# Kernel tuning notes

Measured on AMD Instinct MI355X. Metric: run time of the kernel, lower is better.

The kernel has to match this reference:

```python
import jax, jax.numpy as jnp
import numpy as np

EPS = 0.5  # diffusion epsilon from init_kwargs

def setup_inputs() -> dict:
    key = jax.random.key(0)
    k = jax.random.split(key, 7)
    B, N0, N1, n = 1024, 32, 32, 64
    Mu0 = jax.random.normal(k[0], (N0, n), dtype=jnp.float32) * 2.0
    Mu1 = jax.random.normal(k[1], (N1, n), dtype=jnp.float32) * 2.0
    # diagonal covariances must be positive
    S0 = jax.random.uniform(k[2], (N0, n), dtype=jnp.float32, minval=0.1, maxval=1.0)
    S1 = jax.random.uniform(k[3], (N1, n), dtype=jnp.float32, minval=0.1, maxval=1.0)
    Lam = jax.random.uniform(k[4], (N0, N1), dtype=jnp.float32, minval=0.0, maxval=1.0)
    Lam = Lam / Lam.sum()  # transport plan sums to 1
    X = jax.random.normal(k[5], (B, n), dtype=jnp.float32)
    t = jnp.float32(0.3)
    return {"X": X, "Mu0": Mu0, "Mu1": Mu1, "S0": S0, "S1": S1, "Lam": Lam, "t": t}

def reference(X, Mu0, Mu1, S0, S1, Lam, t):
    eps2 = EPS * EPS
    S0e = S0[:, None, :]        # (N0,1,n)
    S1e = S1[None, :, :]        # (1,N1,n)
    Ds = jnp.sqrt(4.0 * S0e * S1e + EPS ** 4)
    Cs = 0.5 * (Ds - eps2)                       # (N0,N1,n)
    mu_t = (1.0 - t) * Mu0[:, None, :] + t * Mu1[None, :, :]  # (N0,N1,n)
    Sigma = (1.0 - t) ** 2 * S0e + t ** 2 * S1e + 2.0 * t * (1.0 - t) * (Cs + 0.5 * eps2)
    # St = Pt - Qt - eps^2 * t
    St = t * S1e + (1.0 - t) * Cs - ((1.0 - t) * S0e + t * Cs) - eps2 * t
    K = St / Sigma                               # (N0,N1,n)
    v = Mu1[None, :, :] - Mu0[:, None, :]        # (N0,N1,n)
    d = X[:, None, None, :] - mu_t               # (B,N0,N1,n)
    U = K * d + v                                # (B,N0,N1,n)
    # diag-Normal log_prob plus n/2*log(2pi) == -0.5*sum(d^2/Sigma + log Sigma)
    logw = -0.5 * jnp.sum(d * d / Sigma + jnp.log(Sigma), axis=-1)  # (B,N0,N1)
    W = jnp.exp(jnp.clip(logw, -50.0, 50.0)) * Lam                  # (B,N0,N1)
    num = jnp.einsum('bijn,bij->bn', U, W)       # (B,n)
    den = jnp.sum(W, axis=(1, 2))[:, None]       # (B,1)
    return num / den
```

## Files before the change

### kernel.cpp

```cpp
#include <hip/hip_runtime.h>
#include <math.h>

#define EPS2f 0.25f
#define EPS4f 0.0625f

__device__ __forceinline__ float rl(float v, int l) {
    return __int_as_float(__builtin_amdgcn_readlane(__float_as_int(v), l));
}

__global__ __launch_bounds__(256) void precomp_kernel(
    const float* __restrict__ Mu0, const float* __restrict__ Mu1,
    const float* __restrict__ S0,  const float* __restrict__ S1,
    const float* __restrict__ tptr,
    float2* __restrict__ AB2, float2* __restrict__ KV2,
    float* __restrict__ C0)
{
    __shared__ float2 abS[4][67];
    __shared__ float2 kvS[4][64];

    const int tid = threadIdx.x;
    const int k   = tid & 63;
    const int ijl = tid >> 6;
    const int ij0 = blockIdx.x << 2;
    const int ij  = ij0 + ijl;
    const int i   = ij >> 5;
    const int j   = ij & 31;
    const float t   = *tptr;
    const float omt = 1.0f - t;

    const float s0 = S0[i * 64 + k];
    const float s1 = S1[j * 64 + k];
    const float m0 = Mu0[i * 64 + k];
    const float m1 = Mu1[j * 64 + k];

    const float ds  = sqrtf(4.0f * s0 * s1 + EPS4f);
    const float cs  = 0.5f * (ds - EPS2f);
    const float mt  = omt * m0 + t * m1;
    const float sig = omt * omt * s0 + t * t * s1
                    + 2.0f * t * omt * (cs + 0.5f * EPS2f);
    const float isig = 1.0f / sig;
    const float st = t * s1 - omt * s0 + (omt - t) * cs - EPS2f * t;
    const float kk = st * isig;
    const float v  = m1 - m0;

    abS[ijl][k] = make_float2(isig, 2.0f * mt * isig);
    kvS[ijl][k] = make_float2(kk, v - kk * mt);

    float c = mt * mt * isig + __logf(sig);
    #pragma unroll
    for (int off = 32; off >= 1; off >>= 1)
        c += __shfl_xor(c, off, 64);
    if (k == 0) C0[ij] = c;

    __syncthreads();

    {
        const int k2   = tid >> 3;
        const int ijl2 = (tid >> 1) & 3;
        const int par  = tid & 1;
        AB2[(k2 << 11) + ((ij0 + ijl2) << 1) + par] = abS[ijl2][2 * k2 + par];
    }
    {
        const int pr  = tid >> 7;
        const int k6  = (tid >> 1) & 63;
        const int par = tid & 1;
        KV2[(blockIdx.x << 8) + tid] = kvS[(pr << 1) + par][k6];
    }
}

__global__ __launch_bounds__(256) void gmm_main_kernel(
    const float* __restrict__ X,   const float* __restrict__ Lam,
    const float* __restrict__ C0,
    const float4* __restrict__ AB4, const float4* __restrict__ KV4,
    float* __restrict__ nump, float* __restrict__ denp)
{
    const int tid    = threadIdx.x;
    const int lane   = tid & 63;
    const int rowsub = tid >> 6;
    const int bx     = blockIdx.x;
    const int c      = bx & 15;
    const int g      = bx >> 4;
    const int r0     = (g << 5) + (rowsub << 3);
    const int ij     = (c << 6) + lane;

    float xr[8];
    #pragma unroll
    for (int u = 0; u < 8; ++u) xr[u] = X[(r0 + u) * 64 + lane];

    const float c0 = C0[ij];
    const float lm = Lam[ij];

    const float4* __restrict__ abp = AB4 + ij;
    float4 ab[4];
    #pragma unroll
    for (int pf = 0; pf < 4; ++pf) ab[pf] = abp[pf << 10];

    float q[8] = {0.f, 0.f, 0.f, 0.f, 0.f, 0.f, 0.f, 0.f};
    #pragma unroll
    for (int k2 = 0; k2 < 32; ++k2) {
        const float4 a = ab[k2 & 3];
        if (k2 + 4 < 32) ab[k2 & 3] = abp[(k2 + 4) << 10];
        #pragma unroll
        for (int u = 0; u < 8; ++u) {
            const float xe = rl(xr[u], 2 * k2);
            const float xo = rl(xr[u], 2 * k2 + 1);
            q[u] = fmaf(fmaf(a.x, xe, -a.y), xe, q[u]);
            q[u] = fmaf(fmaf(a.z, xo, -a.w), xo, q[u]);
        }
    }

    float wv[8];
    #pragma unroll
    for (int u = 0; u < 8; ++u)
        wv[u] = __expf(fminf(fmaxf(-0.5f * (q[u] + c0), -50.f), 50.f)) * lm;

    const float4* __restrict__ kvp = KV4 + (c << 11) + lane;
    float4 kvb[4];
    #pragma unroll
    for (int pf = 0; pf < 4; ++pf) kvb[pf] = kvp[pf << 6];

    float dsum[8];
    #pragma unroll
    for (int u = 0; u < 8; ++u) dsum[u] = wv[u];
    #pragma unroll
    for (int off = 32; off >= 1; off >>= 1) {
        #pragma unroll
        for (int u = 0; u < 8; ++u) dsum[u] += __shfl_xor(dsum[u], off, 64);
    }

    float nacc[8] = {0.f, 0.f, 0.f, 0.f, 0.f, 0.f, 0.f, 0.f};
    #pragma unroll
    for (int p = 0; p < 32; ++p) {
        const float4 kv = kvb[p & 3];
        if (p + 4 < 32) kvb[p & 3] = kvp[(p + 4) << 6];
        #pragma unroll
        for (int u = 0; u < 8; ++u) {
            const float We = rl(wv[u], 2 * p);
            const float Wo = rl(wv[u], 2 * p + 1);
            const float ue = fmaf(kv.x, xr[u], kv.y);
            nacc[u] = fmaf(We, ue, nacc[u]);
            const float uo = fmaf(kv.z, xr[u], kv.w);
            nacc[u] = fmaf(Wo, uo, nacc[u]);
        }
    }

    #pragma unroll
    for (int u = 0; u < 8; ++u)
        nump[(c * 1024 + r0 + u) * 64 + lane] = nacc[u];

    float dv = dsum[0];
    #pragma unroll
    for (int u = 1; u < 8; ++u) dv = (lane == u) ? dsum[u] : dv;
    if (lane < 8) denp[(c << 10) + r0 + lane] = dv;
}

__global__ __launch_bounds__(256) void combine_kernel(
    const float* __restrict__ nump, const float* __restrict__ denp,
    float* __restrict__ out)
{
    const int idx = blockIdx.x * 256 + threadIdx.x;
    const int b = idx >> 6;
    const int k = idx & 63;
    float s = 0.f, d = 0.f;
    #pragma unroll
    for (int c = 0; c < 16; ++c) {
        s += nump[(c * 1024 + b) * 64 + k];
        d += denp[(c << 10) + b];
    }
    out[idx] = s / d;
}

extern "C" void kernel_launch(void* const* d_in, const int* in_sizes, int n_in,
                              void* d_out, int out_size, void* d_ws, size_t ws_size,
                              hipStream_t stream) {
    const float* X   = (const float*)d_in[0];
    const float* Mu0 = (const float*)d_in[1];
    const float* Mu1 = (const float*)d_in[2];
    const float* S0  = (const float*)d_in[3];
    const float* S1  = (const float*)d_in[4];
    const float* Lam = (const float*)d_in[5];
    const float* t   = (const float*)d_in[6];
    float* out = (float*)d_out;

    char* ws = (char*)d_ws;
    float2* AB2  = (float2*)(ws);
    float2* KV2  = (float2*)(ws + (512 << 10));
    float*  C0   = (float*)(ws + (1024 << 10));
    float*  nump = (float*)(ws + (2 << 20));
    float*  denp = (float*)(ws + (6 << 20));

    precomp_kernel<<<256, 256, 0, stream>>>(Mu0, Mu1, S0, S1, t, AB2, KV2, C0);
    gmm_main_kernel<<<512, 256, 0, stream>>>(X, Lam, C0,
                                             (const float4*)AB2,
                                             (const float4*)KV2, nump, denp);
    combine_kernel<<<256, 256, 0, stream>>>(nump, denp, out);
}
```

Baseline: 85.81 us.

## Fuse precompute, main, and combine kernels into one with last-block reduction

Merges the three launches into a single kernel. Each block recomputes its 64 (i,j) component parameters directly into LDS instead of reading them from a global precompute buffer. The cross-chunk reduction is done by the last block to arrive per row group, tracked with an atomic counter that a memset clears before launch. This removes two kernel launches and the global round trips for AB/KV/C0. In exchange, each parameter set is recomputed by 32 blocks, LDS use grows, and a memset plus threadfence/atomic synchronisation are added.

Result: slower. 144.3 us (+68.2%).

```diff
diff --git a/kernel.cpp b/kernel.cpp
--- a/kernel.cpp
+++ b/kernel.cpp
@@ -8,98 +8,93 @@
     return __int_as_float(__builtin_amdgcn_readlane(__float_as_int(v), l));
 }
 
-__global__ __launch_bounds__(256) void precomp_kernel(
-    const float* __restrict__ Mu0, const float* __restrict__ Mu1,
-    const float* __restrict__ S0,  const float* __restrict__ S1,
+__global__ __launch_bounds__(256, 2) void gmm_chunk_kernel(
+    const float* __restrict__ X,   const float* __restrict__ Mu0,
+    const float* __restrict__ Mu1, const float* __restrict__ S0,
+    const float* __restrict__ S1,  const float* __restrict__ Lam,
     const float* __restrict__ tptr,
-    float2* __restrict__ AB2, float2* __restrict__ KV2,
-    float* __restrict__ C0)
+    float* __restrict__ nump, float* __restrict__ denp,
+    unsigned int* __restrict__ ctr, float* __restrict__ out)
 {
-    __shared__ float2 abS[4][67];
-    __shared__ float2 kvS[4][64];
+    __shared__ float4 abL[32][65];
+    __shared__ float4 kvL[32][65];
+    __shared__ float  c0L[64];
+    __shared__ int    lastFlag;
 
-    const int tid = threadIdx.x;
-    const int k   = tid & 63;
-    const int ijl = tid >> 6;
-    const int ij0 = blockIdx.x << 2;
-    const int ij  = ij0 + ijl;
-    const int i   = ij >> 5;
-    const int j   = ij & 31;
+    const int tid  = threadIdx.x;
+    const int lane = tid & 63;
+    const int w    = tid >> 6;
+    const int g    = blockIdx.x >> 4;
+    const int c    = blockIdx.x & 15;
+    const int r0   = (g << 5) + (w << 3);
+
+    const int m   = tid & 31;
+    const int ijb = (tid >> 5) << 3;
     const float t   = *tptr;
     const float omt = 1.0f - t;
 
-    const float s0 = S0[i * 64 + k];
-    const float s1 = S1[j * 64 + k];
-    const float m0 = Mu0[i * 64 + k];
-    const float m1 = Mu1[j * 64 + k];
-
-    const float ds  = sqrtf(4.0f * s0 * s1 + EPS4f);
-    const float cs  = 0.5f * (ds - EPS2f);
-    const float mt  = omt * m0 + t * m1;
-    const float sig = omt * omt * s0 + t * t * s1
-                    + 2.0f * t * omt * (cs + 0.5f * EPS2f);
-    const float isig = 1.0f / sig;
-    const float st = t * s1 - omt * s0 + (omt - t) * cs - EPS2f * t;
-    const float kk = st * isig;
-    const float v  = m1 - m0;
-
-    abS[ijl][k] = make_float2(isig, 2.0f * mt * isig);
-    kvS[ijl][k] = make_float2(kk, v - kk * mt);
-
-    float c = mt * mt * isig + __logf(sig);
+    float Kr[8][2], Vr[8][2], cpart[8];
     #pragma unroll
-    for (int off = 32; off >= 1; off >>= 1)
-        c += __shfl_xor(c, off, 64);
-    if (k == 0) C0[ij] = c;
-
-    __syncthreads();
-
-    {
-        const int k2   = tid >> 3;
-        const int ijl2 = (tid >> 1) & 3;
-        const int par  = tid & 1;
-        AB2[(k2 << 11) + ((ij0 + ijl2) << 1) + par] = abS[ijl2][2 * k2 + par];
+    for (int v = 0; v < 8; ++v) {
+        const int ij = (c << 6) + ijb + v;
+        const int i  = ij >> 5;
+        const int j  = ij & 31;
+        float4 abv;
+        float  csum = 0.f;
+        #pragma unroll
+        for (int r = 0; r < 2; ++r) {
+            const int k  = 2 * m + r;
+            const float s0 = S0[i * 64 + k];
+            const float s1 = S1[j * 64 + k];
+            const float m0 = Mu0[i * 64 + k];
+            const float m1 = Mu1[j * 64 + k];
+            const float dsq = sqrtf(4.0f * s0 * s1 + EPS4f);
+            const float cs  = 0.5f * (dsq - EPS2f);
+            const float mt  = omt * m0 + t * m1;
+            const float sig = omt * omt * s0 + t * t * s1
+                            + 2.0f * t * omt * (cs + 0.5f * EPS2f);
+            const float isig = 1.0f / sig;
+            const float st  = t * s1 - omt * s0 + (omt - t) * cs - EPS2f * t;
+            const float kk  = st * isig;
+            const float vm  = (m1 - m0) - kk * mt;
+            if (r == 0) { abv.x = isig; abv.y = 2.0f * mt * isig; }
+            else        { abv.z = isig; abv.w = 2.0f * mt * isig; }
+            Kr[v][r] = kk; Vr[v][r] = vm;
+            csum += mt * mt * isig + __logf(sig);
+        }
+        abL[m][ijb + v] = abv;
+        cpart[v] = csum;
     }
-    {
-        const int pr  = tid >> 7;
-        const int k6  = (tid >> 1) & 63;
-        const int par = tid & 1;
-        KV2[(blockIdx.x << 8) + tid] = kvS[(pr << 1) + par][k6];
+    #pragma unroll
+    for (int qq = 0; qq < 4; ++qq) {
+        kvL[(ijb >> 1) + qq][2 * m] =
+            make_float4(Kr[2 * qq][0], Vr[2 * qq][0],
+                        Kr[2 * qq + 1][0], Vr[2 * qq + 1][0]);
+        kvL[(ijb >> 1) + qq][2 * m + 1] =
+            make_float4(Kr[2 * qq][1], Vr[2 * qq][1],
+                        Kr[2 * qq + 1][1], Vr[2 * qq + 1][1]);
     }
-}
-
-__global__ __launch_bounds__(256) void gmm_main_kernel(
-    const float* __restrict__ X,   const float* __restrict__ Lam,
-    const float* __restrict__ C0,
-    const float4* __restrict__ AB4, const float4* __restrict__ KV4,
-    float* __restrict__ nump, float* __restrict__ denp)
-{
-    const int tid    = threadIdx.x;
-    const int lane   = tid & 63;
-    const int rowsub = tid >> 6;
-    const int bx     = blockIdx.x;
-    const int c      = bx & 15;
-    const int g      = bx >> 4;
-    const int r0     = (g << 5) + (rowsub << 3);
-    const int ij     = (c << 6) + lane;
+    #pragma unroll
+    for (int v = 0; v < 8; ++v) {
+        float cc = cpart[v];
+        #pragma unroll
+        for (int off = 16; off >= 1; off >>= 1)
+            cc += __shfl_xor(cc, off, 64);
+        if (m == 0) c0L[ijb + v] = cc;
+    }
 
     float xr[8];
     #pragma unroll
     for (int u = 0; u < 8; ++u) xr[u] = X[(r0 + u) * 64 + lane];
 
-    const float c0 = C0[ij];
-    const float lm = Lam[ij];
+    __syncthreads();
 
-    const float4* __restrict__ abp = AB4 + ij;
-    float4 ab[4];
-    #pragma unroll
-    for (int pf = 0; pf < 4; ++pf) ab[pf] = abp[pf << 10];
-
+    const float c0v = c0L[lane];
+    const float lm  = Lam[(c << 6) + lane];
     float q[8] = {0.f, 0.f, 0.f, 0.f, 0.f, 0.f, 0.f, 0.f};
     #pragma unroll
     for (int k2 = 0; k2 < 32; ++k2) {
-        const float4 a = ab[k2 & 3];
-        if (k2 + 4 < 32) ab[k2 & 3] = abp[(k2 + 4) << 10];
+        const float4 a = abL[k2][lane];
         #pragma unroll
         for (int u = 0; u < 8; ++u) {
             const float xe = rl(xr[u], 2 * k2);
@@ -112,12 +107,7 @@
     float wv[8];
     #pragma unroll
     for (int u = 0; u < 8; ++u)
-        wv[u] = __expf(fminf(fmaxf(-0.5f * (q[u] + c0), -50.f), 50.f)) * lm;
-
-    const float4* __restrict__ kvp = KV4 + (c << 11) + lane;
-    float4 kvb[4];
-    #pragma unroll
-    for (int pf = 0; pf < 4; ++pf) kvb[pf] = kvp[pf << 6];
+        wv[u] = __expf(fminf(fmaxf(-0.5f * (q[u] + c0v), -50.f), 50.f)) * lm;
 
     float dsum[8];
     #pragma unroll
@@ -131,8 +121,7 @@
     float nacc[8] = {0.f, 0.f, 0.f, 0.f, 0.f, 0.f, 0.f, 0.f};
     #pragma unroll
     for (int p = 0; p < 32; ++p) {
-        const float4 kv = kvb[p & 3];
-        if (p + 4 < 32) kvb[p & 3] = kvp[(p + 4) << 6];
+        const float4 kv = kvL[p][lane];
         #pragma unroll
         for (int u = 0; u < 8; ++u) {
             const float We = rl(wv[u], 2 * p);
@@ -144,30 +133,36 @@
         }
     }
 
+    const int b = blockIdx.x;
     #pragma unroll
     for (int u = 0; u < 8; ++u)
-        nump[(c * 1024 + r0 + u) * 64 + lane] = nacc[u];
-
+        nump[(b * 32 + (w << 3) + u) * 64 + lane] = nacc[u];
     float dv = dsum[0];
     #pragma unroll
     for (int u = 1; u < 8; ++u) dv = (lane == u) ? dsum[u] : dv;
-    if (lane < 8) denp[(c << 10) + r0 + lane] = dv;
-}
+    if (lane < 8) denp[b * 32 + (w << 3) + lane] = dv;
 
-__global__ __launch_bounds__(256) void combine_kernel(
-    const float* __restrict__ nump, const float* __restrict__ denp,
-    float* __restrict__ out)
-{
-    const int idx = blockIdx.x * 256 + threadIdx.x;
-    const int b = idx >> 6;
-    const int k = idx & 63;
-    float s = 0.f, d = 0.f;
-    #pragma unroll
-    for (int c = 0; c < 16; ++c) {
-        s += nump[(c * 1024 + b) * 64 + k];
-        d += denp[(c << 10) + b];
+    __threadfence();
+    __syncthreads();
+    if (tid == 0) {
+        const unsigned int old = atomicAdd(&ctr[g], 1u);
+        lastFlag = (old == 15u);
     }
-    out[idx] = s / d;
+    __syncthreads();
+    if (lastFlag) {
+        __threadfence();
+        #pragma unroll
+        for (int u = 0; u < 8; ++u) {
+            const int row = (w << 3) + u;
+            float s = 0.f, d = 0.f;
+            #pragma unroll
+            for (int cc2 = 0; cc2 < 16; ++cc2) {
+                s += nump[((g * 16 + cc2) * 32 + row) * 64 + lane];
+                d += denp[(g * 16 + cc2) * 32 + row];
+            }
+            out[(g * 32 + row) * 64 + lane] = s / d;
+        }
+    }
 }
 
 extern "C" void kernel_launch(void* const* d_in, const int* in_sizes, int n_in,
@@ -183,15 +178,11 @@
     float* out = (float*)d_out;
 
     char* ws = (char*)d_ws;
-    float2* AB2  = (float2*)(ws);
-    float2* KV2  = (float2*)(ws + (512 << 10));
-    float*  C0   = (float*)(ws + (1024 << 10));
-    float*  nump = (float*)(ws + (2 << 20));
-    float*  denp = (float*)(ws + (6 << 20));
+    float*        nump = (float*)(ws);
+    float*        denp = (float*)(ws + (4 << 20));
+    unsigned int* ctr  = (unsigned int*)(ws + (4 << 20) + (64 << 10));
 
-    precomp_kernel<<<256, 256, 0, stream>>>(Mu0, Mu1, S0, S1, t, AB2, KV2, C0);
-    gmm_main_kernel<<<512, 256, 0, stream>>>(X, Lam, C0,
-                                             (const float4*)AB2,
-                                             (const float4*)KV2, nump, denp);
-    combine_kernel<<<256, 256, 0, stream>>>(nump, denp, out);
+    hipMemsetAsync(ctr, 0, 32 * sizeof(unsigned int), stream);
+    gmm_chunk_kernel<<<512, 256, 0, stream>>>(X, Mu0, Mu1, S0, S1, Lam, t,
+                                              nump, denp, ctr, out);
 }
```
